# Kernel tuning notes

Measured on AMD Instinct MI355X. Metric: run time of the kernel, lower is better.

The kernel has to match this reference:

```python
import jax, jax.numpy as jnp
import numpy as np

B, S, D = 4, 2048, 768
H = 12
HD = D // H  # 64


def setup_inputs() -> dict:
    key = jax.random.key(0)
    k1, k2, k3 = jax.random.split(key, 3)
    scale_qkv = (6.0 / (D + 3 * D)) ** 0.5  # xavier_uniform bound
    scale_o = (6.0 / (D + D)) ** 0.5
    return {
        "x": jax.random.normal(k1, (B, S, D), dtype=jnp.float32),
        "w_qkv": jax.random.uniform(k2, (3 * D, D), dtype=jnp.float32, minval=-scale_qkv, maxval=scale_qkv),
        "b_qkv": jnp.zeros((3 * D,), dtype=jnp.float32),
        "w_o": jax.random.uniform(k3, (D, D), dtype=jnp.float32, minval=-scale_o, maxval=scale_o),
        "b_o": jnp.zeros((D,), dtype=jnp.float32),
    }


def reference(x, w_qkv, b_qkv, w_o, b_o):
    b, s, _ = x.shape
    # qkv projection: [B,S,3D]
    qkv = jnp.einsum("bsd,ed->bse", x, w_qkv) + b_qkv
    # [B,S,H,3*HD] -> [B,H,S,3*HD]
    qkv = qkv.reshape(b, s, H, 3 * HD).transpose(0, 2, 1, 3)
    q, k, v = jnp.split(qkv, 3, axis=-1)  # each [B,H,S,HD]
    # scaled dot-product attention (full score matrix, as in source)
    attn_logits = jnp.einsum("bhqd,bhkd->bhqk", q, k) / np.sqrt(HD).astype(np.float32)
    attention = jax.nn.softmax(attn_logits, axis=-1)
    values = jnp.einsum("bhqk,bhkd->bhqd", attention, v)
    # merge heads: [B,S,D]
    values = values.transpose(0, 2, 1, 3).reshape(b, s, D)
    out = jnp.einsum("bsd,ed->bse", values, w_o) + b_o
    return out
```

## Files before the change

kernel.cpp:

```cpp
#include <hip/hip_runtime.h>
#include <hip/hip_bf16.h>

#define BB 4
#define SS 2048
#define DD 768
#define HH 12
#define HDD 64
#define QKVW 2304

typedef _Float16 h8 __attribute__((ext_vector_type(8)));
typedef _Float16 h2 __attribute__((ext_vector_type(2)));
typedef __fp16 fp16x2 __attribute__((ext_vector_type(2)));
typedef float f4 __attribute__((ext_vector_type(4)));

struct __align__(8) Half4 { _Float16 x, y, z, w; };
struct __align__(8) H2x2 { h2 a, b; };

#define QSCALE 0.18033688011112042f
#define SSHIFT -4.0f

__device__ __forceinline__ h2 pk_cvt(float a, float b) {
    fp16x2 r = __builtin_amdgcn_cvt_pkrtz(a, b);
    return __builtin_bit_cast(h2, r);
}

#define N4_X   (BB * SS * DD / 4)
#define N4_WQ  (QKVW * DD / 4)
#define N4_WO  (DD * DD / 4)
#define N4_ALL (N4_X + N4_WQ + N4_WO)

__global__ __launch_bounds__(256) void cvt_all(const float* __restrict__ x,
                                               const float* __restrict__ wq,
                                               const float* __restrict__ wo,
                                               _Float16* __restrict__ xh,
                                               _Float16* __restrict__ wqh,
                                               _Float16* __restrict__ woh) {
    int i = blockIdx.x * 256 + threadIdx.x;
    const float* src;
    _Float16* dst;
    if (i < N4_X) {
        src = x; dst = xh;
    } else if (i < N4_X + N4_WQ) {
        i -= N4_X; src = wq; dst = wqh;
    } else {
        i -= N4_X + N4_WQ; src = wo; dst = woh;
    }
    const float4 v = ((const float4*)src)[i];
    Half4 h = {(_Float16)v.x, (_Float16)v.y, (_Float16)v.z, (_Float16)v.w};
    ((Half4*)dst)[i] = h;
}

__device__ __forceinline__ void gload16(const _Float16* g, _Float16* l) {
    __builtin_amdgcn_global_load_lds(
        (const __attribute__((address_space(1))) unsigned int*)g,
        (__attribute__((address_space(3))) unsigned int*)l, 16, 0, 0);
}

template <int EPI>
__global__ __launch_bounds__(256) void gemm_f16(const _Float16* __restrict__ A,
                                                const _Float16* __restrict__ B,
                                                const float* __restrict__ bias,
                                                float* __restrict__ Cf,
                                                _Float16* __restrict__ Ch,
                                                int M, int N, int K) {
    __shared__ alignas(16) _Float16 Ash[128 * 64];
    __shared__ alignas(16) _Float16 Bsh[128 * 64];

    const int tid = threadIdx.x;
    const int lane = tid & 63;
    const int w = tid >> 6;
    const int l15 = lane & 15;
    const int qd = lane >> 4;
    const int wm = w & 1;
    const int wn = w >> 1;
    const int m0 = blockIdx.y * 128;
    const int n0 = blockIdx.x * 128;
    const int ldsb = w * 512;

    f4 acc[4][4];
#pragma unroll
    for (int mt = 0; mt < 4; ++mt)
#pragma unroll
        for (int nt = 0; nt < 4; ++nt) acc[mt][nt] = (f4){0.f, 0.f, 0.f, 0.f};

    const _Float16* Ab = A + (size_t)m0 * K;
    const _Float16* Bb = B + (size_t)n0 * K;

    const int srow = tid >> 3;
    const int cg = ((tid & 7) ^ (srow & 7)) * 8;
    const int x7 = l15 & 7;

    for (int k0 = 0; k0 < K; k0 += 64) {
        __syncthreads();
#pragma unroll
        for (int i = 0; i < 4; ++i) {
            const size_t gsrc = (size_t)(i * 32 + srow) * K + k0 + cg;
            gload16(Ab + gsrc, Ash + i * 2048 + ldsb);
            gload16(Bb + gsrc, Bsh + i * 2048 + ldsb);
        }
        __syncthreads();

#pragma unroll
        for (int s = 0; s < 2; ++s) {
            h8 aF[4], bF[4];
#pragma unroll
            for (int mt = 0; mt < 4; ++mt)
                aF[mt] = *(const h8*)&Ash[(wm * 64 + mt * 16 + l15) * 64
                                          + (((s * 4 + qd) ^ x7) << 3)];
#pragma unroll
            for (int nt = 0; nt < 4; ++nt)
                bF[nt] = *(const h8*)&Bsh[(wn * 64 + nt * 16 + l15) * 64
                                          + (((s * 4 + qd) ^ x7) << 3)];
#pragma unroll
            for (int mt = 0; mt < 4; ++mt)
#pragma unroll
                for (int nt = 0; nt < 4; ++nt)
                    acc[mt][nt] = __builtin_amdgcn_mfma_f32_16x16x32_f16(
                        bF[nt], aF[mt], acc[mt][nt], 0, 0, 0);
        }
    }

#pragma unroll
    for (int mt = 0; mt < 4; ++mt) {
        const int m = m0 + wm * 64 + mt * 16 + l15;
#pragma unroll
        for (int nt = 0; nt < 4; ++nt) {
            const int nb = n0 + wn * 64 + nt * 16 + qd * 4;
            const float4 bv = *(const float4*)(bias + nb);
            f4 v = acc[mt][nt];
            v[0] += bv.x; v[1] += bv.y; v[2] += bv.z; v[3] += bv.w;
            if (EPI == 0) {
                *(float4*)(Cf + (size_t)m * N + nb) = (float4){v[0], v[1], v[2], v[3]};
            } else {
                if (((nb >> 6) % 3) == 0) {
                    v[0] *= QSCALE; v[1] *= QSCALE; v[2] *= QSCALE; v[3] *= QSCALE;
                }
                H2x2 pk;
                pk.a = pk_cvt(v[0], v[1]);
                pk.b = pk_cvt(v[2], v[3]);
                *(H2x2*)(Ch + (size_t)m * N + nb) = pk;
            }
        }
    }
}

__global__ __launch_bounds__(256, 3) void attn_mfma(const _Float16* __restrict__ qkvh,
                                                    _Float16* __restrict__ vh) {
    __shared__ alignas(16) _Float16 Kh[64 * 64];
    __shared__ alignas(16) _Float16 VT[64 * 64];
    __shared__ alignas(16) _Float16 Psh[4][32 * 72];

    const int tid = threadIdx.x;
    const int lane = tid & 63;
    const int w = tid >> 6;
    const int l15 = lane & 15;
    const int qd = lane >> 4;
    const int h = blockIdx.y;
    const int b = blockIdx.z;
    const int qbase = blockIdx.x * 128 + w * 32;

    const size_t bhrow = (size_t)b * SS;
    const int hcol = h * 192;
    const int x7 = l15 & 7;

    h8 bQ[2][2];
#pragma unroll
    for (int nt = 0; nt < 2; ++nt)
#pragma unroll
        for (int kc = 0; kc < 2; ++kc)
            bQ[nt][kc] = *(const h8*)(qkvh + (bhrow + qbase + nt * 16 + l15) * QKVW
                                      + hcol + kc * 32 + qd * 8);

    f4 O[4][2];
#pragma unroll
    for (int dt = 0; dt < 4; ++dt)
#pragma unroll
        for (int nt = 0; nt < 2; ++nt) O[dt][nt] = (f4){0.f, 0.f, 0.f, 0.f};
    f4 lacc[2] = {(f4){0.f, 0.f, 0.f, 0.f}, (f4){0.f, 0.f, 0.f, 0.f}};

    h8 ones;
#pragma unroll
    for (int i = 0; i < 8; ++i) ones[i] = (_Float16)1.0f;

    _Float16* Pw = &Psh[w][0];

    const int krow = tid >> 3;
    const int kc8 = (tid & 7) * 8;
    const int kpc = (((tid & 7) ^ (krow & 7)) << 3);
    const int vkp = tid & 31;
    const int vc8 = (tid >> 5) * 8;

    h8 kreg[2], vreg[2];
    {
        const _Float16* base = qkvh + (bhrow + 0) * QKVW + hcol;
        kreg[0] = *(const h8*)(base + (size_t)krow * QKVW + 64 + kc8);
        kreg[1] = *(const h8*)(base + (size_t)(32 + krow) * QKVW + 64 + kc8);
        vreg[0] = *(const h8*)(base + (size_t)(2 * vkp) * QKVW + 128 + vc8);
        vreg[1] = *(const h8*)(base + (size_t)(2 * vkp + 1) * QKVW + 128 + vc8);
    }

    for (int kt = 0; kt < SS / 64; ++kt) {
        __syncthreads();
        *(h8*)&Kh[krow * 64 + kpc] = kreg[0];
        *(h8*)&Kh[(32 + krow) * 64 + kpc] = kreg[1];
#pragma unroll
        for (int j = 0; j < 8; ++j) {
            h2 pr = {vreg[0][j], vreg[1][j]};
            *(h2*)&VT[(vc8 + j) * 64 + (((vkp >> 2) ^ j) << 3) + 2 * (vkp & 3)] = pr;
        }
        __syncthreads();

        if (kt + 1 < SS / 64) {
            const _Float16* base = qkvh + (bhrow + (kt + 1) * 64) * QKVW + hcol;
            kreg[0] = *(const h8*)(base + (size_t)krow * QKVW + 64 + kc8);
            kreg[1] = *(const h8*)(base + (size_t)(32 + krow) * QKVW + 64 + kc8);
            vreg[0] = *(const h8*)(base + (size_t)(2 * vkp) * QKVW + 128 + vc8);
            vreg[1] = *(const h8*)(base + (size_t)(2 * vkp + 1) * QKVW + 128 + vc8);
        }

        h8 aK[4][2];
#pragma unroll
        for (int mt = 0; mt < 4; ++mt)
#pragma unroll
            for (int kc = 0; kc < 2; ++kc)
                aK[mt][kc] = *(const h8*)&Kh[(mt * 16 + l15) * 64
                                             + (((kc * 4 + qd) ^ x7) << 3)];

#pragma unroll
        for (int mt = 0; mt < 4; ++mt) {
#pragma unroll
            for (int nt = 0; nt < 2; ++nt) {
                f4 z = (f4){SSHIFT, SSHIFT, SSHIFT, SSHIFT};
                z = __builtin_amdgcn_mfma_f32_16x16x32_f16(aK[mt][0], bQ[nt][0], z, 0, 0, 0);
                z = __builtin_amdgcn_mfma_f32_16x16x32_f16(aK[mt][1], bQ[nt][1], z, 0, 0, 0);
                H2x2 pk;
                pk.a = pk_cvt(exp2f(z[0]), exp2f(z[1]));
                pk.b = pk_cvt(exp2f(z[2]), exp2f(z[3]));
                *(H2x2*)&Pw[(nt * 16 + l15) * 72 + mt * 16 + qd * 4] = pk;
            }
        }

        h8 bP[2][2];
#pragma unroll
        for (int nt = 0; nt < 2; ++nt)
#pragma unroll
            for (int kc = 0; kc < 2; ++kc)
                bP[nt][kc] = *(const h8*)&Pw[(nt * 16 + l15) * 72 + kc * 32 + qd * 8];

#pragma unroll
        for (int nt = 0; nt < 2; ++nt) {
            lacc[nt] = __builtin_amdgcn_mfma_f32_16x16x32_f16(ones, bP[nt][0], lacc[nt], 0, 0, 0);
            lacc[nt] = __builtin_amdgcn_mfma_f32_16x16x32_f16(ones, bP[nt][1], lacc[nt], 0, 0, 0);
        }

        h8 aV[4][2];
#pragma unroll
        for (int dt = 0; dt < 4; ++dt)
#pragma unroll
            for (int kc = 0; kc < 2; ++kc) {
                const int d = dt * 16 + l15;
                aV[dt][kc] = *(const h8*)&VT[d * 64 + (((kc * 4 + qd) ^ (d & 7)) << 3)];
            }
#pragma unroll
        for (int dt = 0; dt < 4; ++dt)
#pragma unroll
            for (int nt = 0; nt < 2; ++nt) {
                O[dt][nt] = __builtin_amdgcn_mfma_f32_16x16x32_f16(aV[dt][0], bP[nt][0], O[dt][nt], 0, 0, 0);
                O[dt][nt] = __builtin_amdgcn_mfma_f32_16x16x32_f16(aV[dt][1], bP[nt][1], O[dt][nt], 0, 0, 0);
            }
    }

#pragma unroll
    for (int nt = 0; nt < 2; ++nt) {
        const float linv = 1.0f / lacc[nt][0];
        const size_t row = bhrow + qbase + nt * 16 + l15;
#pragma unroll
        for (int dt = 0; dt < 4; ++dt) {
            f4 o = O[dt][nt];
            Half4 oh;
            oh.x = (_Float16)(o[0] * linv);
            oh.y = (_Float16)(o[1] * linv);
            oh.z = (_Float16)(o[2] * linv);
            oh.w = (_Float16)(o[3] * linv);
            *(Half4*)(vh + row * DD + h * 64 + dt * 16 + qd * 4) = oh;
        }
    }
}

extern "C" void kernel_launch(void* const* d_in, const int* in_sizes, int n_in,
                              void* d_out, int out_size, void* d_ws, size_t ws_size,
                              hipStream_t stream) {
    const float* x     = (const float*)d_in[0];
    const float* w_qkv = (const float*)d_in[1];
    const float* b_qkv = (const float*)d_in[2];
    const float* w_o   = (const float*)d_in[3];
    const float* b_o   = (const float*)d_in[4];
    float* out = (float*)d_out;

    const int M = BB * SS;

    _Float16* p = (_Float16*)d_ws;
    _Float16* qkv_h = p;  p += (size_t)M * QKVW;
    _Float16* xh = p;     p += (size_t)M * DD;
    _Float16* vh = p;     p += (size_t)M * DD;
    _Float16* wqh = p;    p += (size_t)QKVW * DD;
    _Float16* woh = p;    p += (size_t)DD * DD;

    cvt_all<<<N4_ALL / 256, 256, 0, stream>>>(x, w_qkv, w_o, xh, wqh, woh);

    gemm_f16<1><<<dim3(QKVW / 128, M / 128), 256, 0, stream>>>(
        xh, wqh, b_qkv, nullptr, qkv_h, M, QKVW, DD);

    attn_mfma<<<dim3(SS / 128, HH, BB), 256, 0, stream>>>(qkv_h, vh);

    gemm_f16<0><<<dim3(DD / 128, M / 128), 256, 0, stream>>>(
        vh, woh, b_o, out, nullptr, M, DD, DD);
}
```

Baseline: 250.2 us.

## Write V transposed from QKV GEMM and double-buffer K/V with async LDS loads

The QKV projection epilogue now writes V heads transposed into a separate global buffer, so the attention kernel no longer has to transpose V through registers into LDS. The attention kernel stages K and transposed V straight into double-buffered LDS with global_load_lds and an XOR-swizzled source address. This drops one barrier per tile and overlaps the next tile's load with the current tile's compute. The constant -4 shift applied to the scores before exp2 is also removed. In exchange the GEMM epilogue does scattered 2-byte transposed stores, LDS use doubles (which may hurt occupancy), and removing the shift raises the fp16 overflow risk in the unnormalized exponentials.

```diff
diff --git a/kernel.cpp b/kernel.cpp
--- a/kernel.cpp
+++ b/kernel.cpp
@@ -17,7 +17,6 @@
 struct __align__(8) H2x2 { h2 a, b; };
 
 #define QSCALE 0.18033688011112042f
-#define SSHIFT -4.0f
 
 __device__ __forceinline__ h2 pk_cvt(float a, float b) {
     fp16x2 r = __builtin_amdgcn_cvt_pkrtz(a, b);
@@ -62,6 +61,7 @@
                                                 const float* __restrict__ bias,
                                                 float* __restrict__ Cf,
                                                 _Float16* __restrict__ Ch,
+                                                _Float16* __restrict__ VTg,
                                                 int M, int N, int K) {
     __shared__ alignas(16) _Float16 Ash[128 * 64];
     __shared__ alignas(16) _Float16 Bsh[128 * 64];
@@ -132,22 +132,35 @@
             if (EPI == 0) {
                 *(float4*)(Cf + (size_t)m * N + nb) = (float4){v[0], v[1], v[2], v[3]};
             } else {
-                if (((nb >> 6) % 3) == 0) {
-                    v[0] *= QSCALE; v[1] *= QSCALE; v[2] *= QSCALE; v[3] *= QSCALE;
+                const int typ = (nb >> 6) % 3;
+                if (typ == 2) {
+                    const int h_ = nb / 192;
+                    const int d0 = nb - h_ * 192 - 128;
+                    _Float16* vtp = VTg + ((size_t)(m >> 11) * 768 + h_ * 64 + d0) * 2048
+                                    + (m & 2047);
+                    vtp[0] = (_Float16)v[0];
+                    vtp[2048] = (_Float16)v[1];
+                    vtp[2 * 2048] = (_Float16)v[2];
+                    vtp[3 * 2048] = (_Float16)v[3];
+                } else {
+                    if (typ == 0) {
+                        v[0] *= QSCALE; v[1] *= QSCALE; v[2] *= QSCALE; v[3] *= QSCALE;
+                    }
+                    H2x2 pk;
+                    pk.a = pk_cvt(v[0], v[1]);
+                    pk.b = pk_cvt(v[2], v[3]);
+                    *(H2x2*)(Ch + (size_t)m * N + nb) = pk;
                 }
-                H2x2 pk;
-                pk.a = pk_cvt(v[0], v[1]);
-                pk.b = pk_cvt(v[2], v[3]);
-                *(H2x2*)(Ch + (size_t)m * N + nb) = pk;
             }
         }
     }
 }
 
 __global__ __launch_bounds__(256, 3) void attn_mfma(const _Float16* __restrict__ qkvh,
+                                                    const _Float16* __restrict__ vT,
                                                     _Float16* __restrict__ vh) {
-    __shared__ alignas(16) _Float16 Kh[64 * 64];
-    __shared__ alignas(16) _Float16 VT[64 * 64];
+    __shared__ alignas(16) _Float16 Kh[2][64 * 64];
+    __shared__ alignas(16) _Float16 VTs[2][64 * 64];
     __shared__ alignas(16) _Float16 Psh[4][32 * 72];
 
     const int tid = threadIdx.x;
@@ -184,53 +197,42 @@
 
     _Float16* Pw = &Psh[w][0];
 
-    const int krow = tid >> 3;
-    const int kc8 = (tid & 7) * 8;
-    const int kpc = (((tid & 7) ^ (krow & 7)) << 3);
-    const int vkp = tid & 31;
-    const int vc8 = (tid >> 5) * 8;
-
-    h8 kreg[2], vreg[2];
-    {
-        const _Float16* base = qkvh + (bhrow + 0) * QKVW + hcol;
-        kreg[0] = *(const h8*)(base + (size_t)krow * QKVW + 64 + kc8);
-        kreg[1] = *(const h8*)(base + (size_t)(32 + krow) * QKVW + 64 + kc8);
-        vreg[0] = *(const h8*)(base + (size_t)(2 * vkp) * QKVW + 128 + vc8);
-        vreg[1] = *(const h8*)(base + (size_t)(2 * vkp + 1) * QKVW + 128 + vc8);
-    }
+    const int srow = tid >> 3;
+    const int cgx = ((tid & 7) ^ (srow & 7)) << 3;
+    const _Float16* kgbase = qkvh + bhrow * QKVW + hcol + 64 + cgx;
+    const _Float16* vgbase = vT + ((size_t)b * 768 + h * 64) * 2048 + cgx;
+    const int ldso = w * 512;
+
+    auto stage = [&](int kt, int buf) {
+#pragma unroll
+        for (int i = 0; i < 2; ++i) {
+            gload16(kgbase + (size_t)(kt * 64 + i * 32 + srow) * QKVW,
+                    &Kh[buf][i * 2048 + ldso]);
+            gload16(vgbase + (size_t)(i * 32 + srow) * 2048 + kt * 64,
+                    &VTs[buf][i * 2048 + ldso]);
+        }
+    };
+
+    stage(0, 0);
 
     for (int kt = 0; kt < SS / 64; ++kt) {
+        const int buf = kt & 1;
         __syncthreads();
-        *(h8*)&Kh[krow * 64 + kpc] = kreg[0];
-        *(h8*)&Kh[(32 + krow) * 64 + kpc] = kreg[1];
-#pragma unroll
-        for (int j = 0; j < 8; ++j) {
-            h2 pr = {vreg[0][j], vreg[1][j]};
-            *(h2*)&VT[(vc8 + j) * 64 + (((vkp >> 2) ^ j) << 3) + 2 * (vkp & 3)] = pr;
-        }
-        __syncthreads();
-
-        if (kt + 1 < SS / 64) {
-            const _Float16* base = qkvh + (bhrow + (kt + 1) * 64) * QKVW + hcol;
-            kreg[0] = *(const h8*)(base + (size_t)krow * QKVW + 64 + kc8);
-            kreg[1] = *(const h8*)(base + (size_t)(32 + krow) * QKVW + 64 + kc8);
-            vreg[0] = *(const h8*)(base + (size_t)(2 * vkp) * QKVW + 128 + vc8);
-            vreg[1] = *(const h8*)(base + (size_t)(2 * vkp + 1) * QKVW + 128 + vc8);
-        }
+        if (kt + 1 < SS / 64) stage(kt + 1, buf ^ 1);
 
         h8 aK[4][2];
 #pragma unroll
         for (int mt = 0; mt < 4; ++mt)
 #pragma unroll
             for (int kc = 0; kc < 2; ++kc)
-                aK[mt][kc] = *(const h8*)&Kh[(mt * 16 + l15) * 64
-                                             + (((kc * 4 + qd) ^ x7) << 3)];
+                aK[mt][kc] = *(const h8*)&Kh[buf][(mt * 16 + l15) * 64
+                                                  + (((kc * 4 + qd) ^ x7) << 3)];
 
 #pragma unroll
         for (int mt = 0; mt < 4; ++mt) {
 #pragma unroll
             for (int nt = 0; nt < 2; ++nt) {
-                f4 z = (f4){SSHIFT, SSHIFT, SSHIFT, SSHIFT};
+                f4 z = (f4){0.f, 0.f, 0.f, 0.f};
                 z = __builtin_amdgcn_mfma_f32_16x16x32_f16(aK[mt][0], bQ[nt][0], z, 0, 0, 0);
                 z = __builtin_amdgcn_mfma_f32_16x16x32_f16(aK[mt][1], bQ[nt][1], z, 0, 0, 0);
                 H2x2 pk;
@@ -257,10 +259,9 @@
 #pragma unroll
         for (int dt = 0; dt < 4; ++dt)
 #pragma unroll
-            for (int kc = 0; kc < 2; ++kc) {
-                const int d = dt * 16 + l15;
-                aV[dt][kc] = *(const h8*)&VT[d * 64 + (((kc * 4 + qd) ^ (d & 7)) << 3)];
-            }
+            for (int kc = 0; kc < 2; ++kc)
+                aV[dt][kc] = *(const h8*)&VTs[buf][(dt * 16 + l15) * 64
+                                                   + (((kc * 4 + qd) ^ x7) << 3)];
 #pragma unroll
         for (int dt = 0; dt < 4; ++dt)
 #pragma unroll
@@ -301,6 +302,7 @@
 
     _Float16* p = (_Float16*)d_ws;
     _Float16* qkv_h = p;  p += (size_t)M * QKVW;
+    _Float16* vT = p;     p += (size_t)BB * DD * SS;
     _Float16* xh = p;     p += (size_t)M * DD;
     _Float16* vh = p;     p += (size_t)M * DD;
     _Float16* wqh = p;    p += (size_t)QKVW * DD;
@@ -309,10 +311,10 @@
     cvt_all<<<N4_ALL / 256, 256, 0, stream>>>(x, w_qkv, w_o, xh, wqh, woh);
 
     gemm_f16<1><<<dim3(QKVW / 128, M / 128), 256, 0, stream>>>(
-        xh, wqh, b_qkv, nullptr, qkv_h, M, QKVW, DD);
-
-    attn_mfma<<<dim3(SS / 128, HH, BB), 256, 0, stream>>>(qkv_h, vh);
+        xh, wqh, b_qkv, nullptr, qkv_h, vT, M, QKVW, DD);
+
+    attn_mfma<<<dim3(SS / 128, HH, BB), 256, 0, stream>>>(qkv_h, vT, vh);
 
     gemm_f16<0><<<dim3(DD / 128, M / 128), 256, 0, stream>>>(
-        vh, woh, b_o, out, nullptr, M, DD, DD);
-}
+        vh, woh, b_o, out, nullptr, nullptr, M, DD, DD);
+}
```

Result: no change. 247.0 us (-1.3%).
